# Performance work log

Hardware: AMD Instinct MI355X
Metric: run time of the kernel (lower is better)

The kernel has to match this reference:

```python
import jax, jax.numpy as jnp
import numpy as np

B, I, N, D = 4, 32, 4096, 64
TEM = 1.0
WP = 0.5


def setup_inputs() -> dict:
    key = jax.random.key(0)
    kf, kl = jax.random.split(key)
    x = jax.random.normal(kf, (B, N, D), dtype=jnp.float32)
    # features are L2-normalized ('normed_corr_features')
    x = x / jnp.linalg.norm(x, axis=-1, keepdims=True)
    # assign each correspondence to one of I instances -> boolean masks [B, I, N]
    inst = jax.random.randint(kl, (B, N), 0, I)
    label = (inst[:, None, :] == jnp.arange(I)[None, :, None])  # bool [B, I, N]
    return {"normed_corr_features": x, "label": label}


def reference(normed_corr_features, label):
    x = normed_corr_features                      # [B, N, D]
    m = label.astype(x.dtype)                     # [B, I, N]
    cnt = m.sum(-1)                               # [B, I]
    valid = (cnt >= 5).astype(x.dtype)            # skip instances with <5 points

    sim = jnp.einsum('bpd,bnd->bpn', x, x)        # [B, N, N] full similarity

    # loss_p: mse(sim_p, ones) over the cnt x cnt masked submatrix
    sq = (sim - 1.0) ** 2                         # [B, N, N]
    t = jnp.einsum('bip,bpn->bin', m, sq)         # [B, I, N]
    lp = (t * m).sum(-1) / jnp.maximum(cnt * cnt, 1.0)  # [B, I]

    # loss_n: mean over positive rows p of log(sum over negatives n of exp(sim/tem))
    e = jnp.exp(sim / TEM)                        # [B, N, N]
    s = jnp.einsum('bpn,bin->bip', e, 1.0 - m)    # [B, I, N] row sums over negatives
    ln = (jnp.log(jnp.maximum(s, 1e-30)) * m).sum(-1) / jnp.maximum(cnt, 1.0)  # [B, I]

    denom = jnp.asarray(B * I, x.dtype)
    loss_p = (valid * lp).sum() / denom
    loss_n = (valid * ln).sum() / denom
    return WP * loss_p + (1.0 - WP) * loss_n
```

## Files before the change

kernel.cpp:

```cpp
#include <hip/hip_runtime.h>
#include <stdint.h>

#define Bsz 4
#define Isz 32
#define Nsz 4096
#define Dsz 64
#define WPc 0.5f
#define ALPHA 1.2011224087864498f
#define LN2 0.69314718055994531f
#define LSZ2 256
#define GBLK (Isz * Bsz * 2)

typedef __attribute__((ext_vector_type(8))) short short8;
typedef __attribute__((ext_vector_type(4))) float floatx4;

__device__ inline uint16_t f2bf(float f) {
  uint32_t u = __float_as_uint(f);
  u += 0x7fffu + ((u >> 16) & 1u);
  return (uint16_t)(u >> 16);
}
__device__ inline float exp2_raw(float f) { return __builtin_amdgcn_exp2f(f); }

__global__ __launch_bounds__(256) void prep_kernel(
    const float* __restrict__ x, uint4* __restrict__ xbf,
    float* __restrict__ negtot, float* __restrict__ accum,
    int* __restrict__ ticket) {
  const int gid = blockIdx.x * 256 + threadIdx.x;
  const int m = gid & 15;
  const int quad = (gid >> 4) & 3;
  const int kh = (gid >> 6) & 1;
  const int tile_g = gid >> 7;
  const size_t src = (size_t)(tile_g * 16 + m) * Dsz + kh * 32 + quad * 8;
  const float4 a = *(const float4*)(x + src);
  const float4 c = *(const float4*)(x + src + 4);
  ushort4 lo, hi;
  lo.x = f2bf(a.x * ALPHA); lo.y = f2bf(a.y * ALPHA);
  lo.z = f2bf(a.z * ALPHA); lo.w = f2bf(a.w * ALPHA);
  hi.x = f2bf(c.x * ALPHA); hi.y = f2bf(c.y * ALPHA);
  hi.z = f2bf(c.z * ALPHA); hi.w = f2bf(c.w * ALPHA);
  ushort4* dst = (ushort4*)(xbf + gid);
  dst[0] = lo;
  dst[1] = hi;

  if (blockIdx.x < 64) {
    negtot[gid] = 0.f;
    if (gid == 0) {
      accum[0] = 0.f;
      ticket[0] = 0;
    }
  }
}

__global__ __launch_bounds__(256, 4) void rowsum6_kernel(
    const uint4* __restrict__ xbf, float* __restrict__ negtot) {
  const int t = threadIdx.x;
  const int lane = t & 63;
  const int w = t >> 6;
  const int quad = lane >> 4;
  const int l15 = lane & 15;

  const int b = blockIdx.y;
  const int gw = blockIdx.x * 4 + w;
  const int rg = gw >> 4;
  const int cg = gw & 15;
  const int tb = b * 256;

  short8 af[4][2];
#pragma unroll
  for (int i = 0; i < 4; ++i) {
    const int tile = tb + rg * 4 + i;
#pragma unroll
    for (int kh = 0; kh < 2; ++kh)
      af[i][kh] = *(const short8*)&xbf[(size_t)(tile * 2 + kh) * 64 + lane];
  }

  float negAll[4][4];
#pragma unroll
  for (int i = 0; i < 4; ++i)
#pragma unroll
    for (int r = 0; r < 4; ++r) negAll[i][r] = 0.f;

#pragma unroll 1
  for (int g = 0; g < 8; ++g) {
    short8 bf[2][2];
#pragma unroll
    for (int c = 0; c < 2; ++c) {
      const int tile = tb + cg * 16 + g * 2 + c;
#pragma unroll
      for (int kh = 0; kh < 2; ++kh)
        bf[c][kh] = *(const short8*)&xbf[(size_t)(tile * 2 + kh) * 64 + lane];
    }
    floatx4 acc[4][2];
#pragma unroll
    for (int i = 0; i < 4; ++i)
#pragma unroll
      for (int c = 0; c < 2; ++c) acc[i][c] = (floatx4){0.f, 0.f, 0.f, 0.f};
#pragma unroll
    for (int kh = 0; kh < 2; ++kh)
#pragma unroll
      for (int c = 0; c < 2; ++c)
#pragma unroll
        for (int i = 0; i < 4; ++i)
          acc[i][c] = __builtin_amdgcn_mfma_f32_16x16x32_bf16(
              af[i][kh], bf[c][kh], acc[i][c], 0, 0, 0);
#pragma unroll
    for (int c = 0; c < 2; ++c)
#pragma unroll
      for (int i = 0; i < 4; ++i)
#pragma unroll
        for (int r = 0; r < 4; ++r) negAll[i][r] += exp2_raw(acc[i][c][r]);
  }

  const size_t bN = (size_t)b * Nsz;
  const int wrow0 = rg * 64;
#pragma unroll
  for (int i = 0; i < 4; ++i)
#pragma unroll
    for (int r = 0; r < 4; ++r) {
      float g = negAll[i][r];
#pragma unroll
      for (int m = 1; m < 16; m <<= 1) g += __shfl_xor(g, m, 64);
      if (l15 == 0)
        atomicAdd(&negtot[bN + wrow0 + i * 16 + quad * 4 + r], g);
    }
}

__global__ __launch_bounds__(256) void gram2_kernel(
    const uint4* __restrict__ xbf, const uint8_t* __restrict__ label,
    const float* __restrict__ negtot, float* __restrict__ accum,
    int* __restrict__ ticket, float* __restrict__ out) {
  __shared__ int list[LSZ2];
  __shared__ int scnt;
  __shared__ uint4 grow[LSZ2 * 8];
  __shared__ float sPos[4];
  __shared__ float sLn[4];

  const int t = threadIdx.x;
  const int lane = t & 63;
  const int w = t >> 6;
  const int quad = lane >> 4;
  const int l15 = lane & 15;
  const int i = blockIdx.x;
  const int b = blockIdx.y;
  const int rc = blockIdx.z;
  const size_t bN = (size_t)b * Nsz;
  const int tb = b * 256;

  if (t == 0) scnt = 0;
  __syncthreads();
  {
    const uint4 lv = ((const uint4*)(label + ((size_t)b * Isz + i) * Nsz))[t];
    const uint32_t words[4] = {lv.x, lv.y, lv.z, lv.w};
#pragma unroll
    for (int jw = 0; jw < 4; ++jw)
#pragma unroll
      for (int jb = 0; jb < 4; ++jb) {
        if ((words[jw] >> (jb * 8)) & 0xff) {
          const int idx = atomicAdd(&scnt, 1);
          if (idx < LSZ2) list[idx] = t * 16 + jw * 4 + jb;
        }
      }
  }
  __syncthreads();
  const int cnt = scnt;
  const int cntE = cnt < LSZ2 ? cnt : LSZ2;

  for (int s = t; s < cntE * 8; s += 256) {
    const int j = s >> 3, u = s & 7;
    const int p = list[j];
    const size_t unit =
        (size_t)((tb + (p >> 4)) * 2 + (u >> 2)) * 64 + (u & 3) * 16 + (p & 15);
    grow[(j << 3) | (u ^ (j & 7))] = xbf[unit];
  }
  __syncthreads();

  const bool active = (cnt >= 5) && (rc * 128 < cntE);
  if (active) {
    short8 af[2][2];
#pragma unroll
    for (int rt = 0; rt < 2; ++rt) {
      int ridx = rc * 128 + w * 32 + rt * 16 + l15;
      ridx = ridx < cntE ? ridx : cntE - 1;
#pragma unroll
      for (int kh = 0; kh < 2; ++kh) {
        const int u = quad + kh * 4;
        af[rt][kh] = *(const short8*)&grow[(ridx << 3) | (u ^ (ridx & 7))];
      }
    }

    float pos = 0.f, lns = 0.f;
    float ngrow_acc[2][4] = {{0.f, 0.f, 0.f, 0.f}, {0.f, 0.f, 0.f, 0.f}};
    const int nch = (cntE + 127) >> 7;
    for (int cc = 0; cc < nch; ++cc) {
      short8 bfr[8][2];
      bool cvalid[8];
#pragma unroll
      for (int ct = 0; ct < 8; ++ct) {
        const int cidx0 = cc * 128 + ct * 16 + l15;
        const int cidx = cidx0 < cntE ? cidx0 : cntE - 1;
        cvalid[ct] = cidx0 < cntE;
#pragma unroll
        for (int kh = 0; kh < 2; ++kh) {
          const int u = quad + kh * 4;
          bfr[ct][kh] = *(const short8*)&grow[(cidx << 3) | (u ^ (cidx & 7))];
        }
      }
      floatx4 acc[2][8];
#pragma unroll
      for (int rt = 0; rt < 2; ++rt)
#pragma unroll
        for (int ct = 0; ct < 8; ++ct) acc[rt][ct] = (floatx4){0.f, 0.f, 0.f, 0.f};
#pragma unroll
      for (int kh = 0; kh < 2; ++kh)
#pragma unroll
        for (int ct = 0; ct < 8; ++ct)
#pragma unroll
          for (int rt = 0; rt < 2; ++rt)
            acc[rt][ct] = __builtin_amdgcn_mfma_f32_16x16x32_bf16(
                af[rt][kh], bfr[ct][kh], acc[rt][ct], 0, 0, 0);
#pragma unroll
      for (int rt = 0; rt < 2; ++rt) {
        const int rbase = rc * 128 + w * 32 + rt * 16 + quad * 4;
#pragma unroll
        for (int ct = 0; ct < 8; ++ct) {
#pragma unroll
          for (int r = 0; r < 4; ++r) {
            const bool ok = cvalid[ct] && (rbase + r < cntE);
            const float s = acc[rt][ct][r];
            const float d = __builtin_fmaf(s, LN2, -1.f);
            pos += ok ? d * d : 0.f;
            ngrow_acc[rt][r] += ok ? exp2_raw(s) : 0.f;
          }
        }
      }
    }
#pragma unroll
    for (int rt = 0; rt < 2; ++rt)
#pragma unroll
      for (int r = 0; r < 4; ++r) {
        float g = ngrow_acc[rt][r];
#pragma unroll
        for (int m = 1; m < 16; m <<= 1) g += __shfl_xor(g, m, 64);
        const int ridx = rc * 128 + w * 32 + rt * 16 + quad * 4 + r;
        if (l15 == 0 && ridx < cntE) {
          const float nf = negtot[bN + list[ridx]] - g;
          lns += __logf(fmaxf(nf, 1e-30f));
        }
      }
#pragma unroll
    for (int m = 1; m < 64; m <<= 1) {
      pos += __shfl_xor(pos, m, 64);
      lns += __shfl_xor(lns, m, 64);
    }
    if (lane == 0) {
      sPos[w] = pos;
      sLn[w] = lns;
    }
    __syncthreads();
    if (t == 0) {
      const float pt = sPos[0] + sPos[1] + sPos[2] + sPos[3];
      const float lt = sLn[0] + sLn[1] + sLn[2] + sLn[3];
      const float c = (float)cnt;
      atomicAdd(accum, WPc * pt / (c * c) + (1.f - WPc) * lt / c);
    }
  }
  if (t == 0) {
    __threadfence();
    const int old = atomicAdd(ticket, 1);
    if (old == GBLK - 1) {
      const float tot = atomicAdd(accum, 0.f);
      out[0] = tot / (float)(Bsz * Isz);
    }
  }
}

extern "C" void kernel_launch(void* const* d_in, const int* in_sizes, int n_in,
                              void* d_out, int out_size, void* d_ws,
                              size_t ws_size, hipStream_t stream) {
  const float* x = (const float*)d_in[0];
  const uint8_t* label = (const uint8_t*)d_in[1];
  float* out = (float*)d_out;

  uint4* xbf = (uint4*)d_ws;
  float* negtot = (float*)(xbf + (size_t)Bsz * Nsz * Dsz / 8);
  float* accum = negtot + Bsz * Nsz;
  int* ticket = (int*)(accum + 1);

  prep_kernel<<<512, 256, 0, stream>>>(x, xbf, negtot, accum, ticket);

  dim3 gridA(256, Bsz);
  rowsum6_kernel<<<gridA, 256, 0, stream>>>(xbf, negtot);

  dim3 gridB(Isz, Bsz, 2);
  gram2_kernel<<<gridB, 256, 0, stream>>>(xbf, label, negtot, accum, ticket, out);
}
```

Measured before the change: 84.80 us.

## Exploit Gram matrix symmetry in row-sum kernel to halve MFMA and exp work

The row-sum kernel now computes only the upper/lower triangular 256x256 block pairs of the symmetric similarity matrix. Off-diagonal blocks add their exp values to both row sums and column sums, with the column sums reduced across quads and added atomically. This roughly halves the matmul and exp work. In exchange it adds more atomics on negtot, switches to 64-thread blocks with a triangular index decode, and leaves the work unevenly balanced between diagonal and off-diagonal blocks.

New measurement: 84.92 us. About the same (+0.1%).

```diff
diff --git a/kernel.cpp b/kernel.cpp
--- a/kernel.cpp
+++ b/kernel.cpp
@@ -51,24 +51,36 @@
   }
 }
 
-__global__ __launch_bounds__(256, 4) void rowsum6_kernel(
+__global__ __launch_bounds__(64, 4) void rowsum_sym_kernel(
     const uint4* __restrict__ xbf, float* __restrict__ negtot) {
-  const int t = threadIdx.x;
-  const int lane = t & 63;
-  const int w = t >> 6;
+  const int lane = threadIdx.x;
   const int quad = lane >> 4;
   const int l15 = lane & 15;
 
   const int b = blockIdx.y;
-  const int gw = blockIdx.x * 4 + w;
-  const int rg = gw >> 4;
-  const int cg = gw & 15;
+  const int wu = blockIdx.x;
+  const int st = wu >> 2;
+  const int w = wu & 3;
+
+  int R, C;
+  if (st < 16) {
+    R = st; C = st;
+  } else {
+    const int t = st - 16;
+    int r = (int)((1.0f + sqrtf((float)(8 * t + 1))) * 0.5f);
+    if (r * (r - 1) / 2 > t) --r;
+    else if (r * (r + 1) / 2 <= t) ++r;
+    R = r;
+    C = t - r * (r - 1) / 2;
+  }
+  const bool offdiag = (R != C);
   const int tb = b * 256;
+  const size_t bN = (size_t)b * Nsz;
 
   short8 af[4][2];
 #pragma unroll
   for (int i = 0; i < 4; ++i) {
-    const int tile = tb + rg * 4 + i;
+    const int tile = tb + R * 16 + w * 4 + i;
 #pragma unroll
     for (int kh = 0; kh < 2; ++kh)
       af[i][kh] = *(const short8*)&xbf[(size_t)(tile * 2 + kh) * 64 + lane];
@@ -85,7 +97,7 @@
     short8 bf[2][2];
 #pragma unroll
     for (int c = 0; c < 2; ++c) {
-      const int tile = tb + cg * 16 + g * 2 + c;
+      const int tile = tb + C * 16 + g * 2 + c;
 #pragma unroll
       for (int kh = 0; kh < 2; ++kh)
         bf[c][kh] = *(const short8*)&xbf[(size_t)(tile * 2 + kh) * 64 + lane];
@@ -103,16 +115,37 @@
         for (int i = 0; i < 4; ++i)
           acc[i][c] = __builtin_amdgcn_mfma_f32_16x16x32_bf16(
               af[i][kh], bf[c][kh], acc[i][c], 0, 0, 0);
-#pragma unroll
-    for (int c = 0; c < 2; ++c)
-#pragma unroll
-      for (int i = 0; i < 4; ++i)
-#pragma unroll
-        for (int r = 0; r < 4; ++r) negAll[i][r] += exp2_raw(acc[i][c][r]);
-  }
-
-  const size_t bN = (size_t)b * Nsz;
-  const int wrow0 = rg * 64;
+    if (offdiag) {
+      float colPart[2] = {0.f, 0.f};
+#pragma unroll
+      for (int c = 0; c < 2; ++c)
+#pragma unroll
+        for (int i = 0; i < 4; ++i)
+#pragma unroll
+          for (int r = 0; r < 4; ++r) {
+            const float e = exp2_raw(acc[i][c][r]);
+            negAll[i][r] += e;
+            colPart[c] += e;
+          }
+#pragma unroll
+      for (int c = 0; c < 2; ++c) {
+        float s = colPart[c];
+        s += __shfl_xor(s, 16, 64);
+        s += __shfl_xor(s, 32, 64);
+        if (quad == 0)
+          atomicAdd(&negtot[bN + C * 256 + (g * 2 + c) * 16 + l15], s);
+      }
+    } else {
+#pragma unroll
+      for (int c = 0; c < 2; ++c)
+#pragma unroll
+        for (int i = 0; i < 4; ++i)
+#pragma unroll
+          for (int r = 0; r < 4; ++r) negAll[i][r] += exp2_raw(acc[i][c][r]);
+    }
+  }
+
+  const int wrow0 = R * 256 + w * 64;
 #pragma unroll
   for (int i = 0; i < 4; ++i)
 #pragma unroll
@@ -288,8 +321,8 @@
 
   prep_kernel<<<512, 256, 0, stream>>>(x, xbf, negtot, accum, ticket);
 
-  dim3 gridA(256, Bsz);
-  rowsum6_kernel<<<gridA, 256, 0, stream>>>(xbf, negtot);
+  dim3 gridA(544, Bsz);
+  rowsum_sym_kernel<<<gridA, 64, 0, stream>>>(xbf, negtot);
 
   dim3 gridB(Isz, Bsz, 2);
   gram2_kernel<<<gridB, 256, 0, stream>>>(xbf, label, negtot, accum, ticket, out);
```
